# Optimization experiments

Measured on AMD Instinct MI355X. Metric: run time of the kernel, lower is better.

Reference implementation:

```python
import jax, jax.numpy as jnp
import numpy as np

BLOCK_K = 128  # per_1x128 block quantization: block_n=1 (per row), block_k=128


def _dequant(wq, scale):
    # wq: [E, N, K] quantized codes; scale: [E, N, ceil(K/BLOCK_K)]
    K = wq.shape[-1]
    s_full = jnp.repeat(scale, BLOCK_K, axis=-1)[..., :K]
    return wq * s_full


def setup_inputs() -> dict:
    key = jax.random.key(0)
    ks = jax.random.split(key, 6)
    T, E, H, I = 1024, 8, 1024, 768
    x = jax.random.normal(ks[0], (T, H), dtype=jnp.float32)
    router_logits = jax.random.normal(ks[1], (T, E), dtype=jnp.float32)
    # fp8 codes simulated as float values; block scales positive (scale_inv)
    w13_weight = jax.random.normal(ks[2], (E, 2 * I, H), dtype=jnp.float32) * 0.05
    w13_weight_scale_inv = jax.random.uniform(ks[3], (E, 2 * I, H // BLOCK_K), dtype=jnp.float32, minval=0.5, maxval=1.5)
    w2_weight = jax.random.normal(ks[4], (E, H, I), dtype=jnp.float32) * 0.05
    w2_weight_scale_inv = jax.random.uniform(ks[5], (E, H, I // BLOCK_K), dtype=jnp.float32, minval=0.5, maxval=1.5)
    return {
        "x": x,
        "router_logits": router_logits,
        "w13_weight": w13_weight,
        "w13_weight_scale_inv": w13_weight_scale_inv,
        "w2_weight": w2_weight,
        "w2_weight_scale_inv": w2_weight_scale_inv,
        "top_k": 2,
    }


def reference(x, router_logits, w13_weight, w13_weight_scale_inv, w2_weight, w2_weight_scale_inv, top_k):
    T, H = x.shape
    E = router_logits.shape[-1]
    I = w2_weight.shape[-1]

    # ---- dequantize block-scaled weights (inline dequant of fp8 grouped GEMM) ----
    w13 = _dequant(w13_weight, w13_weight_scale_inv)   # [E, 2I, H]
    w2 = _dequant(w2_weight, w2_weight_scale_inv)      # [E, H, I]

    # ---- routing: softmax scoring, top_k, renormalize ----
    probs = jax.nn.softmax(router_logits, axis=-1)     # [T, E]
    topk_w, topk_idx = jax.lax.top_k(probs, top_k)     # [T, K]
    topk_w = topk_w / jnp.sum(topk_w, axis=-1, keepdims=True)  # renormalize=True
    # dense combine weights [T, E] (scatter of top_k routing weights)
    combine = jnp.zeros((T, E), x.dtype).at[jnp.arange(T)[:, None], topk_idx].add(topk_w)

    # ---- grouped expert FFN (dense-over-experts reference) ----
    gate_up = jnp.einsum('th,enh->ten', x, w13)        # [T, E, 2I]
    gate, up = gate_up[..., :I], gate_up[..., I:]
    act = jax.nn.silu(gate) * up                       # silu activation ('silu')
    out_e = jnp.einsum('tei,ehi->teh', act, w2)        # [T, E, H]

    # ---- combine ----
    return jnp.einsum('teh,te->th', out_e, combine)    # [T, H]
```

## Files before the change

### kernel.cpp

```cpp
#include <hip/hip_runtime.h>

#define T_TOK 1024
#define H_DIM 1024
#define I_DIM 768
#define E_NUM 8

#define A_W13 6144
#define A_X   512
#define A_Z   512
#define G13 1572864
#define G2   786432

#define GEMM1_BLOCKS 1536
#define W2DQ_BLOCKS  3072

#define SLOT 24576
#define A_OFF 16384

typedef __bf16 bf16x8 __attribute__((ext_vector_type(8)));
typedef float  f32x4  __attribute__((ext_vector_type(4)));

__device__ inline bf16x8 cvt8(float4 a, float4 b, float s) {
    bf16x8 o;
    o[0] = (__bf16)(a.x * s); o[1] = (__bf16)(a.y * s);
    o[2] = (__bf16)(a.z * s); o[3] = (__bf16)(a.w * s);
    o[4] = (__bf16)(b.x * s); o[5] = (__bf16)(b.y * s);
    o[6] = (__bf16)(b.z * s); o[7] = (__bf16)(b.w * s);
    return o;
}

__device__ inline void async16(const void* g, void* l) {
    __builtin_amdgcn_global_load_lds(
        (const __attribute__((address_space(1))) unsigned int*)g,
        (__attribute__((address_space(3))) unsigned int*)l, 16, 0, 0);
}

#define VM_WAIT12 asm volatile("s_waitcnt vmcnt(12)" ::: "memory")
#define VM_WAIT6  asm volatile("s_waitcnt vmcnt(6)"  ::: "memory")
#define VM_WAIT0  asm volatile("s_waitcnt vmcnt(0)"  ::: "memory")

__global__ __launch_bounds__(256) void prep13_kernel(
    const float* __restrict__ w13, const float* __restrict__ w13s,
    const float* __restrict__ x,   float4* __restrict__ out4,
    __bf16* __restrict__ w13d,     __bf16* __restrict__ xbf,
    const float* __restrict__ logits,
    int* __restrict__ counts, int* __restrict__ base,
    int* __restrict__ tok_list, float* __restrict__ wt_list)
{
    const int bx = blockIdx.x;
    if (bx < A_W13) {
        int g = bx * 256 + threadIdx.x;
        int k8 = g & 127;
        int row = g >> 7;
        float s = w13s[(row << 3) | (k8 >> 4)];
        const float4* src = (const float4*)w13 + (size_t)g * 2;
        *(bf16x8*)(w13d + (size_t)g * 8) = cvt8(src[0], src[1], s);
        return;
    }
    if (bx < A_W13 + A_X) {
        int g = (bx - A_W13) * 256 + threadIdx.x;
        const float4* src = (const float4*)x + (size_t)g * 2;
        *(bf16x8*)(xbf + (size_t)g * 8) = cvt8(src[0], src[1], 1.0f);
        return;
    }
    if (bx < A_W13 + A_X + A_Z) {
        int go = (bx - A_W13 - A_X) * 256 + threadIdx.x;
        float4 z = make_float4(0.f, 0.f, 0.f, 0.f);
        out4[2 * go] = z; out4[2 * go + 1] = z;
        return;
    }
    __shared__ int cnt[E_NUM];
    const int t0 = threadIdx.x;
    if (t0 < E_NUM) cnt[t0] = 0;
    __syncthreads();
#pragma unroll
    for (int tt = 0; tt < 4; tt++) {
        int t = t0 + tt * 256;
        float l[E_NUM];
#pragma unroll
        for (int e = 0; e < E_NUM; e++) l[e] = logits[t * E_NUM + e];
        int e0 = 0; float m0 = l[0];
#pragma unroll
        for (int e = 1; e < E_NUM; e++) if (l[e] > m0) { m0 = l[e]; e0 = e; }
        int e1 = -1; float m1 = -3e38f;
#pragma unroll
        for (int e = 0; e < E_NUM; e++) if (e != e0 && l[e] > m1) { m1 = l[e]; e1 = e; }
        float w0 = 1.0f / (1.0f + expf(m1 - m0));
        float w1 = 1.0f - w0;
        int p0 = atomicAdd(&cnt[e0], 1);
        tok_list[e0 * T_TOK + p0] = t;
        wt_list[e0 * T_TOK + p0] = w0;
        int p1 = atomicAdd(&cnt[e1], 1);
        tok_list[e1 * T_TOK + p1] = t;
        wt_list[e1 * T_TOK + p1] = w1;
    }
    __syncthreads();
    if (t0 == 0) {
        int s = 0;
        for (int e = 0; e < E_NUM; e++) { base[e] = s; counts[e] = cnt[e]; s += cnt[e]; }
    }
}

#define MFMA(A, B, C) __builtin_amdgcn_mfma_f32_16x16x32_bf16(A, B, C, 0, 0, 0)

struct StgEnt { const char* p; int l; };

__global__ __launch_bounds__(256, 2) void gemm1_kernel(
    const __bf16* __restrict__ xbf,
    const __bf16* __restrict__ w13d,
    const int* __restrict__ counts,
    const int* __restrict__ base,
    const int* __restrict__ tok_list,
    __bf16* __restrict__ act,
    const float* __restrict__ w2,
    const float* __restrict__ w2s,
    __bf16* __restrict__ w2d)
{
    const int bx = blockIdx.x;
    if (bx >= GEMM1_BLOCKS) {
        int g2 = (bx - GEMM1_BLOCKS) * 256 + threadIdx.x;
        unsigned row = (unsigned)g2 / 96u;
        int k8 = g2 - row * 96;
        float s = w2s[row * 6 + (k8 >> 4)];
        const float4* src = (const float4*)w2 + (size_t)g2 * 2;
        *(bf16x8*)(w2d + (size_t)g2 * 8) = cvt8(src[0], src[1], s);
        return;
    }

    const int xcd = bx & 7, t = bx >> 3;
    const int p = t % 12, m = t / 12;
    const int P = xcd + 8 * p;
    const int nb = P % 12, e = P / 12;
    const int count = counts[e];
    const int m0 = m * 64;
    if (m0 >= count) return;
    const int n0 = nb * 64;
    const int abase = base[e];

    __shared__ union { uint4 r4[3 * SLOT / 16]; float gu[64 * 132]; } u;
    __shared__ int tokS[64];
    char* ring = (char*)u.r4;

    const int tid = threadIdx.x;
    if (tid < 64) {
        int r = m0 + tid;
        tokS[tid] = (r < count) ? tok_list[e * T_TOK + r] : tok_list[e * T_TOK];
    }
    __syncthreads();

    const int wv = tid >> 6, ln = tid & 63;
    StgEnt se[6];
#pragma unroll
    for (int j = 0; j < 6; j++) {
        int off = wv * 6144 + j * 1024 + ln * 16;
        se[j].l = wv * 6144 + j * 1024;
        if (off < A_OFF) {
            int r = off >> 7, sl = (off >> 4) & 7, g = sl ^ (r & 7);
            int nB = (r < 64) ? (n0 + r) : (I_DIM + n0 + r - 64);
            se[j].p = (const char*)w13d + ((size_t)e * 2 * I_DIM + nB) * 2048 + g * 16;
        } else {
            int ao = off - A_OFF, r = ao >> 7, sl = (ao >> 4) & 7, g = sl ^ (r & 7);
            se[j].p = (const char*)xbf + (size_t)tokS[r] * 2048 + g * 16;
        }
    }

#define ISSUE(kc, sb) do { \
        async16(se[0].p + (kc) * 128, (sb) + se[0].l); \
        async16(se[1].p + (kc) * 128, (sb) + se[1].l); \
        async16(se[2].p + (kc) * 128, (sb) + se[2].l); \
        async16(se[3].p + (kc) * 128, (sb) + se[3].l); \
        async16(se[4].p + (kc) * 128, (sb) + se[4].l); \
        async16(se[5].p + (kc) * 128, (sb) + se[5].l); } while (0)

    const int wid = wv, lane = ln, lrow = lane & 15, quad = lane >> 4;
    int aoff[2][4], boff[2][2];
#pragma unroll
    for (int kk = 0; kk < 2; kk++) {
        int gph = ((kk * 4 + quad) ^ (lrow & 7)) << 4;
#pragma unroll
        for (int i = 0; i < 4; i++) aoff[kk][i] = (i * 16 + lrow) * 128 + gph;
#pragma unroll
        for (int j = 0; j < 2; j++) boff[kk][j] = (wid * 32 + j * 16 + lrow) * 128 + gph;
    }

    f32x4 acc[4][2];
#pragma unroll
    for (int i = 0; i < 4; i++)
#pragma unroll
        for (int j = 0; j < 2; j++) { f32x4 z = {0.f, 0.f, 0.f, 0.f}; acc[i][j] = z; }

    auto compute = [&](const char* sb) {
        const char* Bb = sb;
        const char* Ab = sb + A_OFF;
#pragma unroll
        for (int kk = 0; kk < 2; kk++) {
            bf16x8 b0 = *(const bf16x8*)(Bb + boff[kk][0]);
            bf16x8 b1 = *(const bf16x8*)(Bb + boff[kk][1]);
#pragma unroll
            for (int i = 0; i < 4; i++) {
                bf16x8 a = *(const bf16x8*)(Ab + aoff[kk][i]);
                acc[i][0] = MFMA(a, b0, acc[i][0]);
                acc[i][1] = MFMA(a, b1, acc[i][1]);
            }
        }
    };

    ISSUE(0, ring);
    ISSUE(1, ring + SLOT);
#pragma unroll
    for (int k = 0; k < 16; k++) {
        if (k + 2 < 16) ISSUE(k + 2, ring + ((k + 2) % 3) * SLOT);
        if (k < 14)       { VM_WAIT12; }
        else if (k == 14) { VM_WAIT6; }
        else              { VM_WAIT0; }
        __builtin_amdgcn_s_barrier();
        compute(ring + (k % 3) * SLOT);
        __builtin_amdgcn_s_barrier();
    }

#pragma unroll
    for (int i = 0; i < 4; i++)
#pragma unroll
        for (int j = 0; j < 2; j++)
#pragma unroll
            for (int r = 0; r < 4; r++) {
                int mr = i * 16 + quad * 4 + r;
                int c = wid * 32 + j * 16 + lrow;
                u.gu[mr * 132 + c] = acc[i][j][r];
            }
    __syncthreads();

#pragma unroll
    for (int ii = 0; ii < 16; ii++) {
        int o = ii * 256 + tid;
        int mr = o >> 6, c = o & 63;
        if (m0 + mr < count) {
            float g  = u.gu[mr * 132 + c];
            float up = u.gu[mr * 132 + 64 + c];
            float a  = g / (1.0f + expf(-g)) * up;
            act[(size_t)(abase + m0 + mr) * I_DIM + n0 + c] = (__bf16)a;
        }
    }
#undef ISSUE
}

__global__ __launch_bounds__(256, 2) void gemm2_kernel(
    const __bf16* __restrict__ act,
    const __bf16* __restrict__ w2d,
    const int* __restrict__ counts,
    const int* __restrict__ base,
    const int* __restrict__ tok_list,
    const float* __restrict__ wt_list,
    float* __restrict__ out)
{
    const int bx = blockIdx.x;
    const int xcd = bx & 7, t = bx >> 3;
    const int p = t & 7, m = t >> 3;
    const int P = xcd + 8 * p;
    const int nb = P & 7, e = P >> 3;
    const int count = counts[e];
    const int m0 = m * 64;
    if (m0 >= count) return;
    const int n0 = nb * 128;
    const int abase = base[e];

    __shared__ uint4 r4[3 * SLOT / 16];
    char* ring = (char*)r4;

    const int tid = threadIdx.x;
    const int wv = tid >> 6, ln = tid & 63;

    StgEnt se[6];
#pragma unroll
    for (int j = 0; j < 6; j++) {
        int off = wv * 6144 + j * 1024 + ln * 16;
        se[j].l = wv * 6144 + j * 1024;
        if (off < A_OFF) {
            int r = off >> 7, sl = (off >> 4) & 7, g = sl ^ (r & 7);
            se[j].p = (const char*)w2d + ((size_t)e * H_DIM + n0 + r) * 1536 + g * 16;
        } else {
            int ao = off - A_OFF, r = ao >> 7, sl = (ao >> 4) & 7, g = sl ^ (r & 7);
            int gr = abase + m0 + r; if (gr > 2 * T_TOK - 1) gr = 2 * T_TOK - 1;
            se[j].p = (const char*)act + (size_t)gr * 1536 + g * 16;
        }
    }

#define ISSUE(kc, sb) do { \
        async16(se[0].p + (kc) * 128, (sb) + se[0].l); \
        async16(se[1].p + (kc) * 128, (sb) + se[1].l); \
        async16(se[2].p + (kc) * 128, (sb) + se[2].l); \
        async16(se[3].p + (kc) * 128, (sb) + se[3].l); \
        async16(se[4].p + (kc) * 128, (sb) + se[4].l); \
        async16(se[5].p + (kc) * 128, (sb) + se[5].l); } while (0)

    const int wid = wv, lane = ln, lrow = lane & 15, quad = lane >> 4;
    int aoff[2][4], boff[2][2];
#pragma unroll
    for (int kk = 0; kk < 2; kk++) {
        int gph = ((kk * 4 + quad) ^ (lrow & 7)) << 4;
#pragma unroll
        for (int i = 0; i < 4; i++) aoff[kk][i] = (i * 16 + lrow) * 128 + gph;
#pragma unroll
        for (int j = 0; j < 2; j++) boff[kk][j] = (wid * 32 + j * 16 + lrow) * 128 + gph;
    }

    f32x4 acc[4][2];
#pragma unroll
    for (int i = 0; i < 4; i++)
#pragma unroll
        for (int j = 0; j < 2; j++) { f32x4 z = {0.f, 0.f, 0.f, 0.f}; acc[i][j] = z; }

    auto compute = [&](const char* sb) {
        const char* Bb = sb;
        const char* Ab = sb + A_OFF;
#pragma unroll
        for (int kk = 0; kk < 2; kk++) {
            bf16x8 b0 = *(const bf16x8*)(Bb + boff[kk][0]);
            bf16x8 b1 = *(const bf16x8*)(Bb + boff[kk][1]);
#pragma unroll
            for (int i = 0; i < 4; i++) {
                bf16x8 a = *(const bf16x8*)(Ab + aoff[kk][i]);
                acc[i][0] = MFMA(a, b0, acc[i][0]);
                acc[i][1] = MFMA(a, b1, acc[i][1]);
            }
        }
    };

    ISSUE(0, ring);
    ISSUE(1, ring + SLOT);
#pragma unroll
    for (int k = 0; k < 12; k++) {
        if (k + 2 < 12) ISSUE(k + 2, ring + ((k + 2) % 3) * SLOT);
        if (k < 10)       { VM_WAIT12; }
        else if (k == 10) { VM_WAIT6; }
        else              { VM_WAIT0; }
        __builtin_amdgcn_s_barrier();
        compute(ring + (k % 3) * SLOT);
        __builtin_amdgcn_s_barrier();
    }

#pragma unroll
    for (int i = 0; i < 4; i++)
#pragma unroll
        for (int r = 0; r < 4; r++) {
            int mr = i * 16 + quad * 4 + r;
            if (m0 + mr < count) {
                int   tk = tok_list[e * T_TOK + m0 + mr];
                float w  = wt_list[e * T_TOK + m0 + mr];
#pragma unroll
                for (int j = 0; j < 2; j++) {
                    int h = n0 + wid * 32 + j * 16 + lrow;
                    atomicAdd(&out[(size_t)tk * H_DIM + h], w * acc[i][j][r]);
                }
            }
        }
#undef ISSUE
}

extern "C" void kernel_launch(void* const* d_in, const int* in_sizes, int n_in,
                              void* d_out, int out_size, void* d_ws, size_t ws_size,
                              hipStream_t stream) {
    (void)in_sizes; (void)n_in; (void)out_size; (void)ws_size;
    const float* x      = (const float*)d_in[0];
    const float* logits = (const float*)d_in[1];
    const float* w13    = (const float*)d_in[2];
    const float* w13s   = (const float*)d_in[3];
    const float* w2     = (const float*)d_in[4];
    const float* w2s    = (const float*)d_in[5];
    float* out = (float*)d_out;

    char* ws = (char*)d_ws;
    int*    counts   = (int*)ws;
    int*    base     = (int*)(ws + 128);
    int*    tok_list = (int*)(ws + 256);
    float*  wt_list  = (float*)(ws + 256 + 32768);
    __bf16* act      = (__bf16*)(ws + 65792);
    __bf16* xbf      = (__bf16*)(ws + 65792 + 3145728);
    __bf16* w13d     = (__bf16*)(ws + 65792 + 3145728 + 2097152);
    __bf16* w2d      = (__bf16*)(ws + 65792 + 3145728 + 2097152 + 25165824);

    prep13_kernel<<<dim3(A_W13 + A_X + A_Z + 1), 256, 0, stream>>>(
        w13, w13s, x, (float4*)out, w13d, xbf,
        logits, counts, base, tok_list, wt_list);
    gemm1_kernel<<<dim3(GEMM1_BLOCKS + W2DQ_BLOCKS), 256, 0, stream>>>(
        xbf, w13d, counts, base, tok_list, act, w2, w2s, w2d);
    gemm2_kernel<<<dim3(1024), 256, 0, stream>>>(
        act, w2d, counts, base, tok_list, wt_list, out);
}
```

Baseline: 154.7 us.

## Fuse weight dequantization into grouped GEMM tile loads, dropping separate dequant passes

Removes the standalone passes that convert w13 and w2 from fp32 to scaled bf16 in workspace. Each GEMM now streams fp32 weight tiles straight into LDS, applies the per-128 block scale and converts to bf16 while building MFMA operands. This avoids writing and re-reading the bf16 weight copies. In exchange the LDS ring shrinks from triple to double buffering, and each B tile is twice as large in fp32, so LDS traffic and conversion work inside the GEMM loop go up.

Result: slower. 159.1 us (+2.9%).

```diff
diff --git a/kernel.cpp b/kernel.cpp
--- a/kernel.cpp
+++ b/kernel.cpp
@@ -5,17 +5,14 @@
 #define I_DIM 768
 #define E_NUM 8
 
-#define A_W13 6144
-#define A_X   512
-#define A_Z   512
-#define G13 1572864
-#define G2   786432
+#define A_X 512
+#define A_Z 512
 
 #define GEMM1_BLOCKS 1536
-#define W2DQ_BLOCKS  3072
-
-#define SLOT 24576
-#define A_OFF 16384
+#define GEMM2_BLOCKS 1024
+
+#define SLOT 40960
+#define A_OFF 32768
 
 typedef __bf16 bf16x8 __attribute__((ext_vector_type(8)));
 typedef float  f32x4  __attribute__((ext_vector_type(4)));
@@ -29,42 +26,40 @@
     return o;
 }
 
+__device__ inline bf16x8 cvt8f(f32x4 a, f32x4 b, float s) {
+    bf16x8 o;
+    o[0] = (__bf16)(a[0] * s); o[1] = (__bf16)(a[1] * s);
+    o[2] = (__bf16)(a[2] * s); o[3] = (__bf16)(a[3] * s);
+    o[4] = (__bf16)(b[0] * s); o[5] = (__bf16)(b[1] * s);
+    o[6] = (__bf16)(b[2] * s); o[7] = (__bf16)(b[3] * s);
+    return o;
+}
+
 __device__ inline void async16(const void* g, void* l) {
     __builtin_amdgcn_global_load_lds(
         (const __attribute__((address_space(1))) unsigned int*)g,
         (__attribute__((address_space(3))) unsigned int*)l, 16, 0, 0);
 }
 
-#define VM_WAIT12 asm volatile("s_waitcnt vmcnt(12)" ::: "memory")
-#define VM_WAIT6  asm volatile("s_waitcnt vmcnt(6)"  ::: "memory")
+#define VM_WAIT10 asm volatile("s_waitcnt vmcnt(10)" ::: "memory")
 #define VM_WAIT0  asm volatile("s_waitcnt vmcnt(0)"  ::: "memory")
 
-__global__ __launch_bounds__(256) void prep13_kernel(
-    const float* __restrict__ w13, const float* __restrict__ w13s,
+__global__ __launch_bounds__(256) void prep_kernel(
     const float* __restrict__ x,   float4* __restrict__ out4,
-    __bf16* __restrict__ w13d,     __bf16* __restrict__ xbf,
+    __bf16* __restrict__ xbf,
     const float* __restrict__ logits,
     int* __restrict__ counts, int* __restrict__ base,
     int* __restrict__ tok_list, float* __restrict__ wt_list)
 {
     const int bx = blockIdx.x;
-    if (bx < A_W13) {
+    if (bx < A_X) {
         int g = bx * 256 + threadIdx.x;
-        int k8 = g & 127;
-        int row = g >> 7;
-        float s = w13s[(row << 3) | (k8 >> 4)];
-        const float4* src = (const float4*)w13 + (size_t)g * 2;
-        *(bf16x8*)(w13d + (size_t)g * 8) = cvt8(src[0], src[1], s);
-        return;
-    }
-    if (bx < A_W13 + A_X) {
-        int g = (bx - A_W13) * 256 + threadIdx.x;
         const float4* src = (const float4*)x + (size_t)g * 2;
         *(bf16x8*)(xbf + (size_t)g * 8) = cvt8(src[0], src[1], 1.0f);
         return;
     }
-    if (bx < A_W13 + A_X + A_Z) {
-        int go = (bx - A_W13 - A_X) * 256 + threadIdx.x;
+    if (bx < A_X + A_Z) {
+        int go = (bx - A_X) * 256 + threadIdx.x;
         float4 z = make_float4(0.f, 0.f, 0.f, 0.f);
         out4[2 * go] = z; out4[2 * go + 1] = z;
         return;
@@ -103,30 +98,16 @@
 
 #define MFMA(A, B, C) __builtin_amdgcn_mfma_f32_16x16x32_bf16(A, B, C, 0, 0, 0)
 
-struct StgEnt { const char* p; int l; };
-
 __global__ __launch_bounds__(256, 2) void gemm1_kernel(
     const __bf16* __restrict__ xbf,
-    const __bf16* __restrict__ w13d,
+    const float* __restrict__ w13,
+    const float* __restrict__ w13s,
     const int* __restrict__ counts,
     const int* __restrict__ base,
     const int* __restrict__ tok_list,
-    __bf16* __restrict__ act,
-    const float* __restrict__ w2,
-    const float* __restrict__ w2s,
-    __bf16* __restrict__ w2d)
+    __bf16* __restrict__ act)
 {
     const int bx = blockIdx.x;
-    if (bx >= GEMM1_BLOCKS) {
-        int g2 = (bx - GEMM1_BLOCKS) * 256 + threadIdx.x;
-        unsigned row = (unsigned)g2 / 96u;
-        int k8 = g2 - row * 96;
-        float s = w2s[row * 6 + (k8 >> 4)];
-        const float4* src = (const float4*)w2 + (size_t)g2 * 2;
-        *(bf16x8*)(w2d + (size_t)g2 * 8) = cvt8(src[0], src[1], s);
-        return;
-    }
-
     const int xcd = bx & 7, t = bx >> 3;
     const int p = t % 12, m = t / 12;
     const int P = xcd + 8 * p;
@@ -137,65 +118,72 @@
     const int n0 = nb * 64;
     const int abase = base[e];
 
-    __shared__ union { uint4 r4[3 * SLOT / 16]; float gu[64 * 132]; } u;
-    __shared__ int tokS[64];
+    __shared__ union { uint4 r4[2 * SLOT / 16]; float gu[64 * 132]; } u;
     char* ring = (char*)u.r4;
 
     const int tid = threadIdx.x;
-    if (tid < 64) {
-        int r = m0 + tid;
-        tokS[tid] = (r < count) ? tok_list[e * T_TOK + r] : tok_list[e * T_TOK];
-    }
-    __syncthreads();
-
     const int wv = tid >> 6, ln = tid & 63;
-    StgEnt se[6];
-#pragma unroll
-    for (int j = 0; j < 6; j++) {
-        int off = wv * 6144 + j * 1024 + ln * 16;
-        se[j].l = wv * 6144 + j * 1024;
-        if (off < A_OFF) {
-            int r = off >> 7, sl = (off >> 4) & 7, g = sl ^ (r & 7);
-            int nB = (r < 64) ? (n0 + r) : (I_DIM + n0 + r - 64);
-            se[j].p = (const char*)w13d + ((size_t)e * 2 * I_DIM + nB) * 2048 + g * 16;
-        } else {
-            int ao = off - A_OFF, r = ao >> 7, sl = (ao >> 4) & 7, g = sl ^ (r & 7);
-            se[j].p = (const char*)xbf + (size_t)tokS[r] * 2048 + g * 16;
-        }
-    }
+
+    const int rE = wv * 32 + (ln >> 4);
+    const int rO = rE + 4;
+    const int gE = (ln & 15) ^ (rE & 7);
+    const int gO = (ln & 15) ^ (rO & 7);
+    auto nbmap = [&](int r) { return (r < 64) ? (n0 + r) : (I_DIM + n0 + r - 64); };
+    const char* pB0 = (const char*)w13 + ((size_t)e * 2 * I_DIM + nbmap(rE)) * 4096 + gE * 16;
+    const char* pB1 = (const char*)w13 + ((size_t)e * 2 * I_DIM + nbmap(rO)) * 4096 + gO * 16;
+    const int rA0 = wv * 16 + (ln >> 3), rA1 = rA0 + 8;
+    const int tk0 = tok_list[e * T_TOK + ((m0 + rA0 < count) ? m0 + rA0 : 0)];
+    const int tk1 = tok_list[e * T_TOK + ((m0 + rA1 < count) ? m0 + rA1 : 0)];
+    const char* pA0 = (const char*)xbf + (size_t)tk0 * 2048 + (((ln & 7) ^ (rA0 & 7)) << 4);
+    const char* pA1 = (const char*)xbf + (size_t)tk1 * 2048 + (((ln & 7) ^ (rA1 & 7)) << 4);
+
+    const int lane = ln, lrow = lane & 15, quad = lane >> 4, wid = wv;
+    const int rB0 = wid * 32 + lrow, rB1 = rB0 + 16;
+    const size_t sB0 = ((size_t)e * 2 * I_DIM + nbmap(rB0)) * 8;
+    const size_t sB1 = ((size_t)e * 2 * I_DIM + nbmap(rB1)) * 8;
+    float scl0[8], scl1[8];
+#pragma unroll
+    for (int kb = 0; kb < 8; kb++) { scl0[kb] = w13s[sB0 + kb]; scl1[kb] = w13s[sB1 + kb]; }
+
+    const int bro0 = rB0 * 256, bro1 = rB1 * 256;
+    const int glo = (((quad * 2) ^ (lrow & 7)) << 4);
+    const int ghi = ((((quad * 2) | 1) ^ (lrow & 7)) << 4);
+    int aoff[2][4];
+#pragma unroll
+    for (int kk = 0; kk < 2; kk++)
+#pragma unroll
+        for (int i = 0; i < 4; i++)
+            aoff[kk][i] = (i * 16 + lrow) * 128 + (((kk * 4 + quad) ^ (lrow & 7)) << 4);
+
+    f32x4 acc[4][2];
+#pragma unroll
+    for (int i = 0; i < 4; i++)
+#pragma unroll
+        for (int j = 0; j < 2; j++) { f32x4 z = {0.f, 0.f, 0.f, 0.f}; acc[i][j] = z; }
 
 #define ISSUE(kc, sb) do { \
-        async16(se[0].p + (kc) * 128, (sb) + se[0].l); \
-        async16(se[1].p + (kc) * 128, (sb) + se[1].l); \
-        async16(se[2].p + (kc) * 128, (sb) + se[2].l); \
-        async16(se[3].p + (kc) * 128, (sb) + se[3].l); \
-        async16(se[4].p + (kc) * 128, (sb) + se[4].l); \
-        async16(se[5].p + (kc) * 128, (sb) + se[5].l); } while (0)
-
-    const int wid = wv, lane = ln, lrow = lane & 15, quad = lane >> 4;
-    int aoff[2][4], boff[2][2];
-#pragma unroll
-    for (int kk = 0; kk < 2; kk++) {
-        int gph = ((kk * 4 + quad) ^ (lrow & 7)) << 4;
-#pragma unroll
-        for (int i = 0; i < 4; i++) aoff[kk][i] = (i * 16 + lrow) * 128 + gph;
-#pragma unroll
-        for (int j = 0; j < 2; j++) boff[kk][j] = (wid * 32 + j * 16 + lrow) * 128 + gph;
-    }
-
-    f32x4 acc[4][2];
-#pragma unroll
-    for (int i = 0; i < 4; i++)
-#pragma unroll
-        for (int j = 0; j < 2; j++) { f32x4 z = {0.f, 0.f, 0.f, 0.f}; acc[i][j] = z; }
-
-    auto compute = [&](const char* sb) {
+        async16(pB0 + (kc) * 256,          (sb) + wv * 8192); \
+        async16(pB1 + (kc) * 256,          (sb) + wv * 8192 + 1024); \
+        async16(pB0 + 32768 + (kc) * 256,  (sb) + wv * 8192 + 2048); \
+        async16(pB1 + 32768 + (kc) * 256,  (sb) + wv * 8192 + 3072); \
+        async16(pB0 + 65536 + (kc) * 256,  (sb) + wv * 8192 + 4096); \
+        async16(pB1 + 65536 + (kc) * 256,  (sb) + wv * 8192 + 5120); \
+        async16(pB0 + 98304 + (kc) * 256,  (sb) + wv * 8192 + 6144); \
+        async16(pB1 + 98304 + (kc) * 256,  (sb) + wv * 8192 + 7168); \
+        async16(pA0 + (kc) * 128,          (sb) + A_OFF + wv * 2048); \
+        async16(pA1 + (kc) * 128,          (sb) + A_OFF + wv * 2048 + 1024); } while (0)
+
+    auto compute = [&](const char* sb, float s0, float s1) {
         const char* Bb = sb;
         const char* Ab = sb + A_OFF;
 #pragma unroll
         for (int kk = 0; kk < 2; kk++) {
-            bf16x8 b0 = *(const bf16x8*)(Bb + boff[kk][0]);
-            bf16x8 b1 = *(const bf16x8*)(Bb + boff[kk][1]);
+            f32x4 l0 = *(const f32x4*)(Bb + bro0 + kk * 128 + glo);
+            f32x4 h0 = *(const f32x4*)(Bb + bro0 + kk * 128 + ghi);
+            f32x4 l1 = *(const f32x4*)(Bb + bro1 + kk * 128 + glo);
+            f32x4 h1 = *(const f32x4*)(Bb + bro1 + kk * 128 + ghi);
+            bf16x8 b0 = cvt8f(l0, h0, s0);
+            bf16x8 b1 = cvt8f(l1, h1, s1);
 #pragma unroll
             for (int i = 0; i < 4; i++) {
                 bf16x8 a = *(const bf16x8*)(Ab + aoff[kk][i]);
@@ -205,18 +193,18 @@
         }
     };
 
+    VM_WAIT0;
     ISSUE(0, ring);
     ISSUE(1, ring + SLOT);
 #pragma unroll
     for (int k = 0; k < 16; k++) {
-        if (k + 2 < 16) ISSUE(k + 2, ring + ((k + 2) % 3) * SLOT);
-        if (k < 14)       { VM_WAIT12; }
-        else if (k == 14) { VM_WAIT6; }
-        else              { VM_WAIT0; }
+        if (k < 15) { VM_WAIT10; } else { VM_WAIT0; }
         __builtin_amdgcn_s_barrier();
-        compute(ring + (k % 3) * SLOT);
+        compute(ring + (k & 1) * SLOT, scl0[k >> 1], scl1[k >> 1]);
         __builtin_amdgcn_s_barrier();
-    }
+        if (k + 2 < 16) ISSUE(k + 2, ring + (k & 1) * SLOT);
+    }
+#undef ISSUE
 
 #pragma unroll
     for (int i = 0; i < 4; i++)
@@ -241,12 +229,12 @@
             act[(size_t)(abase + m0 + mr) * I_DIM + n0 + c] = (__bf16)a;
         }
     }
-#undef ISSUE
 }
 
 __global__ __launch_bounds__(256, 2) void gemm2_kernel(
     const __bf16* __restrict__ act,
-    const __bf16* __restrict__ w2d,
+    const float* __restrict__ w2,
+    const float* __restrict__ w2s,
     const int* __restrict__ counts,
     const int* __restrict__ base,
     const int* __restrict__ tok_list,
@@ -264,59 +252,71 @@
     const int n0 = nb * 128;
     const int abase = base[e];
 
-    __shared__ uint4 r4[3 * SLOT / 16];
+    __shared__ uint4 r4[2 * SLOT / 16];
     char* ring = (char*)r4;
 
     const int tid = threadIdx.x;
     const int wv = tid >> 6, ln = tid & 63;
 
-    StgEnt se[6];
-#pragma unroll
-    for (int j = 0; j < 6; j++) {
-        int off = wv * 6144 + j * 1024 + ln * 16;
-        se[j].l = wv * 6144 + j * 1024;
-        if (off < A_OFF) {
-            int r = off >> 7, sl = (off >> 4) & 7, g = sl ^ (r & 7);
-            se[j].p = (const char*)w2d + ((size_t)e * H_DIM + n0 + r) * 1536 + g * 16;
-        } else {
-            int ao = off - A_OFF, r = ao >> 7, sl = (ao >> 4) & 7, g = sl ^ (r & 7);
-            int gr = abase + m0 + r; if (gr > 2 * T_TOK - 1) gr = 2 * T_TOK - 1;
-            se[j].p = (const char*)act + (size_t)gr * 1536 + g * 16;
-        }
-    }
+    const int rE = wv * 32 + (ln >> 4);
+    const int rO = rE + 4;
+    const int gE = (ln & 15) ^ (rE & 7);
+    const int gO = (ln & 15) ^ (rO & 7);
+    const char* pB0 = (const char*)w2 + ((size_t)e * H_DIM + n0 + rE) * 3072 + gE * 16;
+    const char* pB1 = (const char*)w2 + ((size_t)e * H_DIM + n0 + rO) * 3072 + gO * 16;
+    const int rA0 = wv * 16 + (ln >> 3), rA1 = rA0 + 8;
+    int gr0 = abase + m0 + rA0; if (gr0 > 2 * T_TOK - 1) gr0 = 2 * T_TOK - 1;
+    int gr1 = abase + m0 + rA1; if (gr1 > 2 * T_TOK - 1) gr1 = 2 * T_TOK - 1;
+    const char* pA0 = (const char*)act + (size_t)gr0 * 1536 + (((ln & 7) ^ (rA0 & 7)) << 4);
+    const char* pA1 = (const char*)act + (size_t)gr1 * 1536 + (((ln & 7) ^ (rA1 & 7)) << 4);
+
+    const int lane = ln, lrow = lane & 15, quad = lane >> 4, wid = wv;
+    const int rB0 = wid * 32 + lrow, rB1 = rB0 + 16;
+    const size_t sB0 = ((size_t)e * H_DIM + n0 + rB0) * 6;
+    const size_t sB1 = ((size_t)e * H_DIM + n0 + rB1) * 6;
+    float scl0[6], scl1[6];
+#pragma unroll
+    for (int kb = 0; kb < 6; kb++) { scl0[kb] = w2s[sB0 + kb]; scl1[kb] = w2s[sB1 + kb]; }
+
+    const int bro0 = rB0 * 256, bro1 = rB1 * 256;
+    const int glo = (((quad * 2) ^ (lrow & 7)) << 4);
+    const int ghi = ((((quad * 2) | 1) ^ (lrow & 7)) << 4);
+    int aoff[2][4];
+#pragma unroll
+    for (int kk = 0; kk < 2; kk++)
+#pragma unroll
+        for (int i = 0; i < 4; i++)
+            aoff[kk][i] = (i * 16 + lrow) * 128 + (((kk * 4 + quad) ^ (lrow & 7)) << 4);
+
+    f32x4 acc[4][2];
+#pragma unroll
+    for (int i = 0; i < 4; i++)
+#pragma unroll
+        for (int j = 0; j < 2; j++) { f32x4 z = {0.f, 0.f, 0.f, 0.f}; acc[i][j] = z; }
 
 #define ISSUE(kc, sb) do { \
-        async16(se[0].p + (kc) * 128, (sb) + se[0].l); \
-        async16(se[1].p + (kc) * 128, (sb) + se[1].l); \
-        async16(se[2].p + (kc) * 128, (sb) + se[2].l); \
-        async16(se[3].p + (kc) * 128, (sb) + se[3].l); \
-        async16(se[4].p + (kc) * 128, (sb) + se[4].l); \
-        async16(se[5].p + (kc) * 128, (sb) + se[5].l); } while (0)
-
-    const int wid = wv, lane = ln, lrow = lane & 15, quad = lane >> 4;
-    int aoff[2][4], boff[2][2];
-#pragma unroll
-    for (int kk = 0; kk < 2; kk++) {
-        int gph = ((kk * 4 + quad) ^ (lrow & 7)) << 4;
-#pragma unroll
-        for (int i = 0; i < 4; i++) aoff[kk][i] = (i * 16 + lrow) * 128 + gph;
-#pragma unroll
-        for (int j = 0; j < 2; j++) boff[kk][j] = (wid * 32 + j * 16 + lrow) * 128 + gph;
-    }
-
-    f32x4 acc[4][2];
-#pragma unroll
-    for (int i = 0; i < 4; i++)
-#pragma unroll
-        for (int j = 0; j < 2; j++) { f32x4 z = {0.f, 0.f, 0.f, 0.f}; acc[i][j] = z; }
-
-    auto compute = [&](const char* sb) {
+        async16(pB0 + (kc) * 256,          (sb) + wv * 8192); \
+        async16(pB1 + (kc) * 256,          (sb) + wv * 8192 + 1024); \
+        async16(pB0 + 24576 + (kc) * 256,  (sb) + wv * 8192 + 2048); \
+        async16(pB1 + 24576 + (kc) * 256,  (sb) + wv * 8192 + 3072); \
+        async16(pB0 + 49152 + (kc) * 256,  (sb) + wv * 8192 + 4096); \
+        async16(pB1 + 49152 + (kc) * 256,  (sb) + wv * 8192 + 5120); \
+        async16(pB0 + 73728 + (kc) * 256,  (sb) + wv * 8192 + 6144); \
+        async16(pB1 + 73728 + (kc) * 256,  (sb) + wv * 8192 + 7168); \
+        async16(pA0 + (kc) * 128,          (sb) + A_OFF + wv * 2048); \
+        async16(pA1 + (kc) * 128,          (sb) + A_OFF + wv * 2048 + 1024); } while (0)
+
+    auto compute = [&](const char* sb, float s0, float s1) {
         const char* Bb = sb;
         const char* Ab = sb + A_OFF;
 #pragma unroll
         for (int kk = 0; kk < 2; kk++) {
-            bf16x8 b0 = *(const bf16x8*)(Bb + boff[kk][0]);
-            bf16x8 b1 = *(const bf16x8*)(Bb + boff[kk][1]);
+            f32x4 l0 = *(const f32x4*)(Bb + bro0 + kk * 128 + glo);
+            f32x4 h0 = *(const f32x4*)(Bb + bro0 + kk * 128 + ghi);
+            f32x4 l1 = *(const f32x4*)(Bb + bro1 + kk * 128 + glo);
+            f32x4 h1 = *(const f32x4*)(Bb + bro1 + kk * 128 + ghi);
+            bf16x8 b0 = cvt8f(l0, h0, s0);
+            bf16x8 b1 = cvt8f(l1, h1, s1);
 #pragma unroll
             for (int i = 0; i < 4; i++) {
                 bf16x8 a = *(const bf16x8*)(Ab + aoff[kk][i]);
@@ -326,18 +326,18 @@
         }
     };
 
+    VM_WAIT0;
     ISSUE(0, ring);
     ISSUE(1, ring + SLOT);
 #pragma unroll
     for (int k = 0; k < 12; k++) {
-        if (k + 2 < 12) ISSUE(k + 2, ring + ((k + 2) % 3) * SLOT);
-        if (k < 10)       { VM_WAIT12; }
-        else if (k == 10) { VM_WAIT6; }
-        else              { VM_WAIT0; }
+        if (k < 11) { VM_WAIT10; } else { VM_WAIT0; }
         __builtin_amdgcn_s_barrier();
-        compute(ring + (k % 3) * SLOT);
+        compute(ring + (k & 1) * SLOT, scl0[k >> 1], scl1[k >> 1]);
         __builtin_amdgcn_s_barrier();
-    }
+        if (k + 2 < 12) ISSUE(k + 2, ring + (k & 1) * SLOT);
+    }
+#undef ISSUE
 
 #pragma unroll
     for (int i = 0; i < 4; i++)
@@ -354,7 +354,6 @@
                 }
             }
         }
-#undef ISSUE
 }
 
 extern "C" void kernel_launch(void* const* d_in, const int* in_sizes, int n_in,
@@ -376,14 +375,11 @@
     float*  wt_list  = (float*)(ws + 256 + 32768);
     __bf16* act      = (__bf16*)(ws + 65792);
     __bf16* xbf      = (__bf16*)(ws + 65792 + 3145728);
-    __bf16* w13d     = (__bf16*)(ws + 65792 + 3145728 + 2097152);
-    __bf16* w2d      = (__bf16*)(ws + 65792 + 3145728 + 2097152 + 25165824);
-
-    prep13_kernel<<<dim3(A_W13 + A_X + A_Z + 1), 256, 0, stream>>>(
-        w13, w13s, x, (float4*)out, w13d, xbf,
-        logits, counts, base, tok_list, wt_list);
-    gemm1_kernel<<<dim3(GEMM1_BLOCKS + W2DQ_BLOCKS), 256, 0, stream>>>(
-        xbf, w13d, counts, base, tok_list, act, w2, w2s, w2d);
-    gemm2_kernel<<<dim3(1024), 256, 0, stream>>>(
-        act, w2d, counts, base, tok_list, wt_list, out);
-}
+
+    prep_kernel<<<dim3(A_X + A_Z + 1), 256, 0, stream>>>(
+        x, (float4*)out, xbf, logits, counts, base, tok_list, wt_list);
+    gemm1_kernel<<<dim3(GEMM1_BLOCKS), 256, 0, stream>>>(
+        xbf, w13, w13s, counts, base, tok_list, act);
+    gemm2_kernel<<<dim3(GEMM2_BLOCKS), 256, 0, stream>>>(
+        act, w2, w2s, counts, base, tok_list, wt_list, out);
+}
```

## Fuse MoE prep, gate-up GEMM and down GEMM into one cooperative persistent kernel

Applied to the files above, without the earlier changes.

Replaces the three separate launches with a single cooperative kernel of 512 persistent blocks that runs dequant/convert/zero plus routing, then the gate-up GEMM, then the down GEMM, separated by grid-wide syncs. The w2 dequant moves from the gemm1 launch into the initial prep phase, and each phase loops over the original block indices. This is meant to remove launch gaps and tail effects between kernels. In exchange the grid syncs serialize the phases, so w2 dequant no longer overlaps with gemm1, and a three-kernel fallback runs if the cooperative launch fails.

Result: slower. 290.8 us (+88.0%).

```diff
diff --git a/kernel.cpp b/kernel.cpp
--- a/kernel.cpp
+++ b/kernel.cpp
@@ -1,24 +1,31 @@
 #include <hip/hip_runtime.h>
+#include <hip/hip_cooperative_groups.h>
+
+namespace cg = cooperative_groups;
 
 #define T_TOK 1024
 #define H_DIM 1024
 #define I_DIM 768
 #define E_NUM 8
-
-#define A_W13 6144
-#define A_X   512
-#define A_Z   512
+#define NBLK  512
+
 #define G13 1572864
 #define G2   786432
-
-#define GEMM1_BLOCKS 1536
-#define W2DQ_BLOCKS  3072
+#define GX   131072
+#define GZ   131072
+#define GTOT (G13 + G2 + GX + GZ)
 
 #define SLOT 24576
 #define A_OFF 16384
 
 typedef __bf16 bf16x8 __attribute__((ext_vector_type(8)));
 typedef float  f32x4  __attribute__((ext_vector_type(4)));
+
+typedef struct {
+    union { uint4 r4[3 * SLOT / 16]; float gu[64 * 132]; } u;
+    int tokS[64];
+    int cnt[E_NUM];
+} SharedBlk;
 
 __device__ inline bf16x8 cvt8(float4 a, float4 b, float s) {
     bf16x8 o;
@@ -39,43 +46,58 @@
 #define VM_WAIT6  asm volatile("s_waitcnt vmcnt(6)"  ::: "memory")
 #define VM_WAIT0  asm volatile("s_waitcnt vmcnt(0)"  ::: "memory")
 
-__global__ __launch_bounds__(256) void prep13_kernel(
+#define MFMA(A, B, C) __builtin_amdgcn_mfma_f32_16x16x32_bf16(A, B, C, 0, 0, 0)
+
+struct StgEnt { const char* p; int l; };
+
+__device__ __forceinline__ void phase0_dev(
+    int bid, int tid,
+    const float* __restrict__ x,
     const float* __restrict__ w13, const float* __restrict__ w13s,
-    const float* __restrict__ x,   float4* __restrict__ out4,
-    __bf16* __restrict__ w13d,     __bf16* __restrict__ xbf,
+    const float* __restrict__ w2,  const float* __restrict__ w2s,
+    float* __restrict__ out,
+    __bf16* __restrict__ w13d, __bf16* __restrict__ w2d, __bf16* __restrict__ xbf)
+{
+    float4* out4 = (float4*)out;
+#pragma unroll
+    for (int uu = 0; uu < 20; uu++) {
+        int g = uu * (NBLK * 256) + bid * 256 + tid;
+        if (g < G13) {
+            int k8 = g & 127;
+            int row = g >> 7;
+            float s = w13s[(row << 3) | (k8 >> 4)];
+            const float4* src = (const float4*)w13 + (size_t)g * 2;
+            *(bf16x8*)(w13d + (size_t)g * 8) = cvt8(src[0], src[1], s);
+        } else if (g < G13 + G2) {
+            int g2 = g - G13;
+            unsigned row = (unsigned)g2 / 96u;
+            int k8 = g2 - row * 96;
+            float s = w2s[row * 6 + (k8 >> 4)];
+            const float4* src = (const float4*)w2 + (size_t)g2 * 2;
+            *(bf16x8*)(w2d + (size_t)g2 * 8) = cvt8(src[0], src[1], s);
+        } else if (g < G13 + G2 + GX) {
+            int gx = g - (G13 + G2);
+            const float4* src = (const float4*)x + (size_t)gx * 2;
+            *(bf16x8*)(xbf + (size_t)gx * 8) = cvt8(src[0], src[1], 1.0f);
+        } else {
+            int go = g - (G13 + G2 + GX);
+            float4 z = make_float4(0.f, 0.f, 0.f, 0.f);
+            out4[2 * go] = z; out4[2 * go + 1] = z;
+        }
+    }
+}
+
+__device__ __forceinline__ void router_dev(
+    int tid, int* cnt,
     const float* __restrict__ logits,
     int* __restrict__ counts, int* __restrict__ base,
     int* __restrict__ tok_list, float* __restrict__ wt_list)
 {
-    const int bx = blockIdx.x;
-    if (bx < A_W13) {
-        int g = bx * 256 + threadIdx.x;
-        int k8 = g & 127;
-        int row = g >> 7;
-        float s = w13s[(row << 3) | (k8 >> 4)];
-        const float4* src = (const float4*)w13 + (size_t)g * 2;
-        *(bf16x8*)(w13d + (size_t)g * 8) = cvt8(src[0], src[1], s);
-        return;
-    }
-    if (bx < A_W13 + A_X) {
-        int g = (bx - A_W13) * 256 + threadIdx.x;
-        const float4* src = (const float4*)x + (size_t)g * 2;
-        *(bf16x8*)(xbf + (size_t)g * 8) = cvt8(src[0], src[1], 1.0f);
-        return;
-    }
-    if (bx < A_W13 + A_X + A_Z) {
-        int go = (bx - A_W13 - A_X) * 256 + threadIdx.x;
-        float4 z = make_float4(0.f, 0.f, 0.f, 0.f);
-        out4[2 * go] = z; out4[2 * go + 1] = z;
-        return;
-    }
-    __shared__ int cnt[E_NUM];
-    const int t0 = threadIdx.x;
-    if (t0 < E_NUM) cnt[t0] = 0;
+    if (tid < E_NUM) cnt[tid] = 0;
     __syncthreads();
 #pragma unroll
     for (int tt = 0; tt < 4; tt++) {
-        int t = t0 + tt * 256;
+        int t = tid + tt * 256;
         float l[E_NUM];
 #pragma unroll
         for (int e = 0; e < E_NUM; e++) l[e] = logits[t * E_NUM + e];
@@ -95,38 +117,18 @@
         wt_list[e1 * T_TOK + p1] = w1;
     }
     __syncthreads();
-    if (t0 == 0) {
+    if (tid == 0) {
         int s = 0;
         for (int e = 0; e < E_NUM; e++) { base[e] = s; counts[e] = cnt[e]; s += cnt[e]; }
     }
 }
 
-#define MFMA(A, B, C) __builtin_amdgcn_mfma_f32_16x16x32_bf16(A, B, C, 0, 0, 0)
-
-struct StgEnt { const char* p; int l; };
-
-__global__ __launch_bounds__(256, 2) void gemm1_kernel(
-    const __bf16* __restrict__ xbf,
-    const __bf16* __restrict__ w13d,
-    const int* __restrict__ counts,
-    const int* __restrict__ base,
-    const int* __restrict__ tok_list,
-    __bf16* __restrict__ act,
-    const float* __restrict__ w2,
-    const float* __restrict__ w2s,
-    __bf16* __restrict__ w2d)
-{
-    const int bx = blockIdx.x;
-    if (bx >= GEMM1_BLOCKS) {
-        int g2 = (bx - GEMM1_BLOCKS) * 256 + threadIdx.x;
-        unsigned row = (unsigned)g2 / 96u;
-        int k8 = g2 - row * 96;
-        float s = w2s[row * 6 + (k8 >> 4)];
-        const float4* src = (const float4*)w2 + (size_t)g2 * 2;
-        *(bf16x8*)(w2d + (size_t)g2 * 8) = cvt8(src[0], src[1], s);
-        return;
-    }
-
+__device__ __forceinline__ void phase1_dev(
+    int bx, int tid, SharedBlk* sh,
+    const __bf16* __restrict__ xbf, const __bf16* __restrict__ w13d,
+    const int* __restrict__ counts, const int* __restrict__ base,
+    const int* __restrict__ tok_list, __bf16* __restrict__ act)
+{
     const int xcd = bx & 7, t = bx >> 3;
     const int p = t % 12, m = t / 12;
     const int P = xcd + 8 * p;
@@ -136,15 +138,11 @@
     if (m0 >= count) return;
     const int n0 = nb * 64;
     const int abase = base[e];
-
-    __shared__ union { uint4 r4[3 * SLOT / 16]; float gu[64 * 132]; } u;
-    __shared__ int tokS[64];
-    char* ring = (char*)u.r4;
-
-    const int tid = threadIdx.x;
+    char* ring = (char*)sh->u.r4;
+
     if (tid < 64) {
         int r = m0 + tid;
-        tokS[tid] = (r < count) ? tok_list[e * T_TOK + r] : tok_list[e * T_TOK];
+        sh->tokS[tid] = (r < count) ? tok_list[e * T_TOK + r] : tok_list[e * T_TOK];
     }
     __syncthreads();
 
@@ -160,11 +158,11 @@
             se[j].p = (const char*)w13d + ((size_t)e * 2 * I_DIM + nB) * 2048 + g * 16;
         } else {
             int ao = off - A_OFF, r = ao >> 7, sl = (ao >> 4) & 7, g = sl ^ (r & 7);
-            se[j].p = (const char*)xbf + (size_t)tokS[r] * 2048 + g * 16;
-        }
-    }
-
-#define ISSUE(kc, sb) do { \
+            se[j].p = (const char*)xbf + (size_t)sh->tokS[r] * 2048 + g * 16;
+        }
+    }
+
+#define ISSUE1(kc, sb) do { \
         async16(se[0].p + (kc) * 128, (sb) + se[0].l); \
         async16(se[1].p + (kc) * 128, (sb) + se[1].l); \
         async16(se[2].p + (kc) * 128, (sb) + se[2].l); \
@@ -205,11 +203,12 @@
         }
     };
 
-    ISSUE(0, ring);
-    ISSUE(1, ring + SLOT);
+    VM_WAIT0;
+    ISSUE1(0, ring);
+    ISSUE1(1, ring + SLOT);
 #pragma unroll
     for (int k = 0; k < 16; k++) {
-        if (k + 2 < 16) ISSUE(k + 2, ring + ((k + 2) % 3) * SLOT);
+        if (k + 2 < 16) ISSUE1(k + 2, ring + ((k + 2) % 3) * SLOT);
         if (k < 14)       { VM_WAIT12; }
         else if (k == 14) { VM_WAIT6; }
         else              { VM_WAIT0; }
@@ -217,6 +216,7 @@
         compute(ring + (k % 3) * SLOT);
         __builtin_amdgcn_s_barrier();
     }
+#undef ISSUE1
 
 #pragma unroll
     for (int i = 0; i < 4; i++)
@@ -226,7 +226,7 @@
             for (int r = 0; r < 4; r++) {
                 int mr = i * 16 + quad * 4 + r;
                 int c = wid * 32 + j * 16 + lrow;
-                u.gu[mr * 132 + c] = acc[i][j][r];
+                sh->u.gu[mr * 132 + c] = acc[i][j][r];
             }
     __syncthreads();
 
@@ -235,25 +235,22 @@
         int o = ii * 256 + tid;
         int mr = o >> 6, c = o & 63;
         if (m0 + mr < count) {
-            float g  = u.gu[mr * 132 + c];
-            float up = u.gu[mr * 132 + 64 + c];
+            float g  = sh->u.gu[mr * 132 + c];
+            float up = sh->u.gu[mr * 132 + 64 + c];
             float a  = g / (1.0f + expf(-g)) * up;
             act[(size_t)(abase + m0 + mr) * I_DIM + n0 + c] = (__bf16)a;
         }
     }
-#undef ISSUE
-}
-
-__global__ __launch_bounds__(256, 2) void gemm2_kernel(
-    const __bf16* __restrict__ act,
-    const __bf16* __restrict__ w2d,
-    const int* __restrict__ counts,
-    const int* __restrict__ base,
-    const int* __restrict__ tok_list,
-    const float* __restrict__ wt_list,
+    __syncthreads();
+}
+
+__device__ __forceinline__ void phase2_dev(
+    int bx, int tid, SharedBlk* sh,
+    const __bf16* __restrict__ act, const __bf16* __restrict__ w2d,
+    const int* __restrict__ counts, const int* __restrict__ base,
+    const int* __restrict__ tok_list, const float* __restrict__ wt_list,
     float* __restrict__ out)
 {
-    const int bx = blockIdx.x;
     const int xcd = bx & 7, t = bx >> 3;
     const int p = t & 7, m = t >> 3;
     const int P = xcd + 8 * p;
@@ -263,13 +260,9 @@
     if (m0 >= count) return;
     const int n0 = nb * 128;
     const int abase = base[e];
-
-    __shared__ uint4 r4[3 * SLOT / 16];
-    char* ring = (char*)r4;
-
-    const int tid = threadIdx.x;
+    char* ring = (char*)sh->u.r4;
+
     const int wv = tid >> 6, ln = tid & 63;
-
     StgEnt se[6];
 #pragma unroll
     for (int j = 0; j < 6; j++) {
@@ -285,7 +278,7 @@
         }
     }
 
-#define ISSUE(kc, sb) do { \
+#define ISSUE2(kc, sb) do { \
         async16(se[0].p + (kc) * 128, (sb) + se[0].l); \
         async16(se[1].p + (kc) * 128, (sb) + se[1].l); \
         async16(se[2].p + (kc) * 128, (sb) + se[2].l); \
@@ -326,11 +319,12 @@
         }
     };
 
-    ISSUE(0, ring);
-    ISSUE(1, ring + SLOT);
+    VM_WAIT0;
+    ISSUE2(0, ring);
+    ISSUE2(1, ring + SLOT);
 #pragma unroll
     for (int k = 0; k < 12; k++) {
-        if (k + 2 < 12) ISSUE(k + 2, ring + ((k + 2) % 3) * SLOT);
+        if (k + 2 < 12) ISSUE2(k + 2, ring + ((k + 2) % 3) * SLOT);
         if (k < 10)       { VM_WAIT12; }
         else if (k == 10) { VM_WAIT6; }
         else              { VM_WAIT0; }
@@ -338,6 +332,7 @@
         compute(ring + (k % 3) * SLOT);
         __builtin_amdgcn_s_barrier();
     }
+#undef ISSUE2
 
 #pragma unroll
     for (int i = 0; i < 4; i++)
@@ -354,7 +349,63 @@
                 }
             }
         }
-#undef ISSUE
+}
+
+__global__ __launch_bounds__(256, 2) void moe_fused(
+    const float* __restrict__ x, const float* __restrict__ logits,
+    const float* __restrict__ w13, const float* __restrict__ w13s,
+    const float* __restrict__ w2, const float* __restrict__ w2s,
+    float* __restrict__ out,
+    int* counts, int* base, int* tok_list, float* wt_list,
+    __bf16* act, __bf16* xbf, __bf16* w13d, __bf16* w2d)
+{
+    cg::grid_group grid = cg::this_grid();
+    __shared__ SharedBlk sh;
+    const int bid = blockIdx.x, tid = threadIdx.x;
+
+    phase0_dev(bid, tid, x, w13, w13s, w2, w2s, out, w13d, w2d, xbf);
+    if (bid == 0) router_dev(tid, sh.cnt, logits, counts, base, tok_list, wt_list);
+    grid.sync();
+
+    for (int it = 0; it < 3; ++it)
+        phase1_dev(bid + NBLK * it, tid, &sh, xbf, w13d, counts, base, tok_list, act);
+    grid.sync();
+
+    for (int it = 0; it < 2; ++it)
+        phase2_dev(bid + NBLK * it, tid, &sh, act, w2d, counts, base, tok_list, wt_list, out);
+}
+
+__global__ __launch_bounds__(256) void fb_prep(
+    const float* __restrict__ x, const float* __restrict__ logits,
+    const float* __restrict__ w13, const float* __restrict__ w13s,
+    const float* __restrict__ w2, const float* __restrict__ w2s,
+    float* __restrict__ out,
+    int* counts, int* base, int* tok_list, float* wt_list,
+    __bf16* xbf, __bf16* w13d, __bf16* w2d)
+{
+    __shared__ int cnt[E_NUM];
+    phase0_dev(blockIdx.x, threadIdx.x, x, w13, w13s, w2, w2s, out, w13d, w2d, xbf);
+    if (blockIdx.x == 0)
+        router_dev(threadIdx.x, cnt, logits, counts, base, tok_list, wt_list);
+}
+
+__global__ __launch_bounds__(256, 2) void fb_gemm1(
+    const __bf16* __restrict__ xbf, const __bf16* __restrict__ w13d,
+    const int* __restrict__ counts, const int* __restrict__ base,
+    const int* __restrict__ tok_list, __bf16* __restrict__ act)
+{
+    __shared__ SharedBlk sh;
+    phase1_dev(blockIdx.x, threadIdx.x, &sh, xbf, w13d, counts, base, tok_list, act);
+}
+
+__global__ __launch_bounds__(256, 2) void fb_gemm2(
+    const __bf16* __restrict__ act, const __bf16* __restrict__ w2d,
+    const int* __restrict__ counts, const int* __restrict__ base,
+    const int* __restrict__ tok_list, const float* __restrict__ wt_list,
+    float* __restrict__ out)
+{
+    __shared__ SharedBlk sh;
+    phase2_dev(blockIdx.x, threadIdx.x, &sh, act, w2d, counts, base, tok_list, wt_list, out);
 }
 
 extern "C" void kernel_launch(void* const* d_in, const int* in_sizes, int n_in,
@@ -379,11 +430,19 @@
     __bf16* w13d     = (__bf16*)(ws + 65792 + 3145728 + 2097152);
     __bf16* w2d      = (__bf16*)(ws + 65792 + 3145728 + 2097152 + 25165824);
 
-    prep13_kernel<<<dim3(A_W13 + A_X + A_Z + 1), 256, 0, stream>>>(
-        w13, w13s, x, (float4*)out, w13d, xbf,
-        logits, counts, base, tok_list, wt_list);
-    gemm1_kernel<<<dim3(GEMM1_BLOCKS + W2DQ_BLOCKS), 256, 0, stream>>>(
-        xbf, w13d, counts, base, tok_list, act, w2, w2s, w2d);
-    gemm2_kernel<<<dim3(1024), 256, 0, stream>>>(
-        act, w2d, counts, base, tok_list, wt_list, out);
-}
+    void* kargs[] = { (void*)&x, (void*)&logits, (void*)&w13, (void*)&w13s,
+                      (void*)&w2, (void*)&w2s, (void*)&out,
+                      (void*)&counts, (void*)&base, (void*)&tok_list, (void*)&wt_list,
+                      (void*)&act, (void*)&xbf, (void*)&w13d, (void*)&w2d };
+    hipError_t err = hipLaunchCooperativeKernel(
+        (const void*)moe_fused, dim3(NBLK), dim3(256), kargs, 0, stream);
+    if (err != hipSuccess) {
+        fb_prep<<<dim3(NBLK), 256, 0, stream>>>(
+            x, logits, w13, w13s, w2, w2s, out,
+            counts, base, tok_list, wt_list, xbf, w13d, w2d);
+        fb_gemm1<<<dim3(1536), 256, 0, stream>>>(
+            xbf, w13d, counts, base, tok_list, act);
+        fb_gemm2<<<dim3(1024), 256, 0, stream>>>(
+            act, w2d, counts, base, tok_list, wt_list, out);
+    }
+}
```
